# Kernel tuning notes

Measured on AMD Instinct MI355X. Metric: run time of the kernel, lower is better.

Reference implementation:

```python
import jax, jax.numpy as jnp
import numpy as np

N_EMBD = 1024
HEAD_SIZE = 64


def setup_inputs() -> dict:
    key = jax.random.key(0)
    kx, kq, kk, kv = jax.random.split(key, 4)
    B, T = 8, 2048
    x = jax.random.normal(kx, (B, T, N_EMBD), dtype=jnp.float32)
    s = 1.0 / np.sqrt(N_EMBD)
    Wq = jax.random.normal(kq, (N_EMBD, HEAD_SIZE), dtype=jnp.float32) * s
    Wk = jax.random.normal(kk, (N_EMBD, HEAD_SIZE), dtype=jnp.float32) * s
    Wv = jax.random.normal(kv, (N_EMBD, HEAD_SIZE), dtype=jnp.float32) * s
    return {"x": x, "Wq": Wq, "Wk": Wk, "Wv": Wv}


def reference(x, Wq, Wk, Wv):
    # x: [B, T, C]; W*: [C, H]
    q = jnp.einsum('btc,ch->bth', x, Wq)
    k = jnp.einsum('btc,ch->bth', x, Wk)
    v = jnp.einsum('btc,ch->bth', x, Wv)
    H = q.shape[-1]
    score = jnp.einsum('bth,bsh->bts', q, k) / jnp.sqrt(jnp.asarray(H, q.dtype))
    T = score.shape[-1]
    causal = jnp.tril(jnp.ones((T, T), dtype=bool))  # [T, T]
    score = jnp.where(causal, score, -jnp.inf)
    attn = jax.nn.softmax(score, axis=-1)
    return jnp.einsum('bts,bsh->bth', attn, v)
```

## Files before the change

kernel.cpp:

```cpp
#include <hip/hip_runtime.h>

typedef __bf16 bf16;
typedef __attribute__((ext_vector_type(8))) __bf16 bf16x8;
typedef __attribute__((ext_vector_type(4))) __bf16 bf16x4;
typedef __attribute__((ext_vector_type(4))) float floatx4;

#define MFMA16(a, b, c) __builtin_amdgcn_mfma_f32_16x16x32_bf16((a), (b), (c), 0, 0, 0)

__global__ void prep_w(const float* __restrict__ Wq, const float* __restrict__ Wk,
                       const float* __restrict__ Wv, bf16* __restrict__ wTf) {
    int tid = blockIdx.x * 256 + threadIdx.x;
    int j = tid & 7;
    int l = (tid >> 3) & 15;
    int q = (tid >> 7) & 3;
    int kc = (tid >> 9) & 31;
    int mt = tid >> 14;
    int mat = mt >> 2;
    int h = ((mt & 3) << 4) + l;
    int c = kc * 32 + q * 8 + j;
    const float* W = (mat == 0) ? Wq : (mat == 1) ? Wk : Wv;
    wTf[tid] = (bf16)W[c * 64 + h];
}

__global__ __launch_bounds__(256, 2) void proj_qkv(const float* __restrict__ x,
                                                   const bf16* __restrict__ wTf,
                                                   bf16* __restrict__ q,
                                                   bf16* __restrict__ k,
                                                   bf16* __restrict__ vT) {
    __shared__ __align__(16) char xsb[32 * 2048];

    const int tid = threadIdx.x;
    const int lane = tid & 63;
    const int w = tid >> 6;
    const int l15 = lane & 15;
    const int quad = lane >> 4;
    const int T0 = blockIdx.x * 32;

    const int srow = tid >> 3;
    const int scg = tid & 7;
    const float* sg = x + (size_t)(T0 + srow) * 1024 + scg * 8;
    char* sld = xsb + srow * 2048;
    const int sws = (srow & 7) << 4;

#define STC(c, f0, f1)                                                          \
    {                                                                            \
        bf16x8 pk;                                                               \
        pk[0] = (bf16)(f0)[0]; pk[1] = (bf16)(f0)[1];                            \
        pk[2] = (bf16)(f0)[2]; pk[3] = (bf16)(f0)[3];                            \
        pk[4] = (bf16)(f1)[0]; pk[5] = (bf16)(f1)[1];                            \
        pk[6] = (bf16)(f1)[2]; pk[7] = (bf16)(f1)[3];                            \
        *(bf16x8*)(sld + (((c) * 128 + scg * 16) ^ sws)) = pk;                   \
    }

    floatx4 A0 = *(const floatx4*)(sg);
    floatx4 A1 = *(const floatx4*)(sg + 4);
    floatx4 B0 = *(const floatx4*)(sg + 64);
    floatx4 B1 = *(const floatx4*)(sg + 68);
    floatx4 C0 = *(const floatx4*)(sg + 128);
    floatx4 C1 = *(const floatx4*)(sg + 132);
    STC(0, A0, A1);
    __syncthreads();

    floatx4 acc[6] = {};
    const bf16* aw0 = wTf + (size_t)(w * 3 + 0) * 16384 + lane * 8;
    const bf16* aw1 = wTf + (size_t)(w * 3 + 1) * 16384 + lane * 8;
    const bf16* aw2 = wTf + (size_t)(w * 3 + 2) * 16384 + lane * 8;
    const char* xr = xsb + l15 * 2048;
    const int sx = (l15 & 7) << 4;
    const int q16 = quad * 16;

    bf16x8 a0c = *(const bf16x8*)(aw0);
    bf16x8 a1c = *(const bf16x8*)(aw1);
    bf16x8 a2c = *(const bf16x8*)(aw2);
    bf16x8 a0n = *(const bf16x8*)(aw0 + 512);
    bf16x8 a1n = *(const bf16x8*)(aw1 + 512);
    bf16x8 a2n = *(const bf16x8*)(aw2 + 512);

    #pragma unroll
    for (int c = 0; c < 16; c++) {
        floatx4 N0 = {}, N1 = {};
        if (c < 13) {
            N0 = *(const floatx4*)(sg + (c + 3) * 64);
            N1 = *(const floatx4*)(sg + (c + 3) * 64 + 4);
        }
        #pragma unroll
        for (int u = 0; u < 2; u++) {
            const int kc = 2 * c + u;
            bf16x8 p0 = *(const bf16x8*)(aw0 + (kc + 2) * 512);
            bf16x8 p1 = *(const bf16x8*)(aw1 + (kc + 2) * 512);
            bf16x8 p2 = *(const bf16x8*)(aw2 + (kc + 2) * 512);
            const int o = (kc * 64 + q16) ^ sx;
            bf16x8 b0 = *(const bf16x8*)(xr + o);
            bf16x8 b1 = *(const bf16x8*)(xr + 32768 + o);
            acc[0] = MFMA16(a0c, b0, acc[0]);
            acc[1] = MFMA16(a0c, b1, acc[1]);
            acc[2] = MFMA16(a1c, b0, acc[2]);
            acc[3] = MFMA16(a1c, b1, acc[3]);
            acc[4] = MFMA16(a2c, b0, acc[4]);
            acc[5] = MFMA16(a2c, b1, acc[5]);
            a0c = a0n; a1c = a1n; a2c = a2n;
            a0n = p0;  a1n = p1;  a2n = p2;
        }
        if (c < 15) STC(c + 1, B0, B1);
        __syncthreads();
        B0 = C0; B1 = C1; C0 = N0; C1 = N1;
    }
#undef STC

    #pragma unroll
    for (int i = 0; i < 3; i++) {
        int mtile = w * 3 + i;
        int mat = mtile >> 2;
        int hbase = ((mtile & 3) << 4) + (quad << 2);
        float sc = (mat == 0) ? 0.18033688011112042f : 1.0f;
        #pragma unroll
        for (int tt = 0; tt < 2; tt++) {
            const int t = T0 + tt * 16 + l15;
            floatx4 av = acc[i * 2 + tt];
            bf16x4 pk;
            pk[0] = (bf16)(av[0] * sc);
            pk[1] = (bf16)(av[1] * sc);
            pk[2] = (bf16)(av[2] * sc);
            pk[3] = (bf16)(av[3] * sc);
            if (mat == 0) {
                *(bf16x4*)(q + (size_t)t * 64 + hbase) = pk;
            } else if (mat == 1) {
                *(bf16x4*)(k + (size_t)t * 64 + hbase) = pk;
            } else {
                int bidx = t >> 11, tmod = t & 2047;
                #pragma unroll
                for (int r = 0; r < 4; r++)
                    vT[(size_t)(bidx * 64 + hbase + r) * 2048 + tmod] = pk[r];
            }
        }
    }
}

#define KP2 72
#define OH 68

__global__ __launch_bounds__(512, 4) void flash(const bf16* __restrict__ q,
                                                const bf16* __restrict__ k,
                                                const bf16* __restrict__ vT,
                                                float* __restrict__ out) {
    __shared__ char smem[8 * 16 * OH * 4];
    __shared__ float Ms[8][16], Ls[8][16];
    bf16* psall = (bf16*)smem;
    float* Os = (float*)smem;

    const int b = blockIdx.x & 7;
    const int p = blockIdx.x >> 3;
    const int t0A = p * 16;
    const int t0B = (127 - p) * 16;
    const int nttA = (p >> 2) + 1;
    const int nttB = ((127 - p) >> 2) + 1;
    const int L = nttA + nttB;

    const int tid = threadIdx.x;
    const int w = tid >> 6;
    const int lane = tid & 63;
    const int l15 = lane & 15;
    const int quad = lane >> 4;

    const int s0 = (L * w) >> 3;
    const int s1 = (L * (w + 1)) >> 3;

    const bf16* kbase = k + (size_t)(b * 2048 + l15) * 64 + quad * 8;
    const bf16* vbase = vT + (size_t)(b * 64 + l15) * 2048 + quad * 8;
    bf16* psw = psall + w * 16 * KP2;

    const bf16* qpA = q + (size_t)(b * 2048 + t0A + l15) * 64 + quad * 8;
    const bf16* qpB = q + (size_t)(b * 2048 + t0B + l15) * 64 + quad * 8;

    floatx4 oA[4] = {}, oB[4] = {};
    float miA = -1e30f, liA = 0.f, miB = -1e30f, liB = 0.f;

#define KV_STEP(jtv, isdiag, t0v, qf0v, qf1v, mi_, li_, o_)                          \
    {                                                                                 \
        const bf16* kp = kbase + (size_t)(jtv) * 4096;                                \
        floatx4 stt[4];                                                               \
        __builtin_amdgcn_s_setprio(1);                                                \
        _Pragma("unroll") for (int mt = 0; mt < 4; mt++) {                            \
            floatx4 z = {};                                                           \
            bf16x8 ka0 = *(const bf16x8*)(kp + mt * 1024);                            \
            bf16x8 ka1 = *(const bf16x8*)(kp + mt * 1024 + 32);                       \
            z = MFMA16(ka0, qf0v, z);                                                 \
            z = MFMA16(ka1, qf1v, z);                                                 \
            stt[mt] = z;                                                              \
        }                                                                             \
        __builtin_amdgcn_s_setprio(0);                                                \
        if (isdiag) {                                                                 \
            _Pragma("unroll") for (int mt = 0; mt < 4; mt++)                          \
                _Pragma("unroll") for (int r = 0; r < 4; r++) {                       \
                    int kv = (jtv) * 64 + mt * 16 + quad * 4 + r;                     \
                    if (kv > (t0v) + l15) stt[mt][r] = -1e30f;                        \
                }                                                                     \
        }                                                                             \
        float m0_ = fmaxf(fmaxf(stt[0][0], stt[0][1]), stt[0][2]);                    \
        float m1_ = fmaxf(fmaxf(stt[0][3], stt[1][0]), stt[1][1]);                    \
        float m2_ = fmaxf(fmaxf(stt[1][2], stt[1][3]), stt[2][0]);                    \
        float m3_ = fmaxf(fmaxf(stt[2][1], stt[2][2]), stt[2][3]);                    \
        float m4_ = fmaxf(fmaxf(stt[3][0], stt[3][1]), stt[3][2]);                    \
        float mx = fmaxf(fmaxf(fmaxf(m0_, m1_), m2_),                                 \
                         fmaxf(fmaxf(m3_, m4_), stt[3][3]));                          \
        mx = fmaxf(mx, __shfl_xor(mx, 16, 64));                                       \
        mx = fmaxf(mx, __shfl_xor(mx, 32, 64));                                       \
        const bool nodefer = !__all(mx - mi_ <= 8.0f);                                \
        const float mnew = nodefer ? fmaxf(mi_, mx) : mi_;                            \
        float rs = 0.f;                                                               \
        _Pragma("unroll") for (int mt = 0; mt < 4; mt++)                              \
            _Pragma("unroll") for (int r = 0; r < 4; r++) {                           \
                float pv = __builtin_amdgcn_exp2f(stt[mt][r] - mnew);                 \
                stt[mt][r] = pv;                                                      \
                rs += pv;                                                             \
            }                                                                         \
        rs += __shfl_xor(rs, 16, 64);                                                 \
        rs += __shfl_xor(rs, 32, 64);                                                 \
        if (nodefer) {                                                                \
            const float aa = __builtin_amdgcn_exp2f(mi_ - mnew);                      \
            mi_ = mnew;                                                               \
            li_ *= aa;                                                                \
            _Pragma("unroll") for (int mt = 0; mt < 4; mt++)                          \
                _Pragma("unroll") for (int r = 0; r < 4; r++) o_[mt][r] *= aa;        \
        }                                                                             \
        li_ += rs;                                                                    \
        _Pragma("unroll") for (int mt = 0; mt < 4; mt++) {                            \
            bf16x4 pk;                                                                \
            pk[0] = (bf16)stt[mt][0]; pk[1] = (bf16)stt[mt][1];                       \
            pk[2] = (bf16)stt[mt][2]; pk[3] = (bf16)stt[mt][3];                       \
            *(bf16x4*)(psw + l15 * KP2 + mt * 16 + quad * 4) = pk;                    \
        }                                                                             \
        const bf16* vp = vbase + (jtv) * 64;                                          \
        __builtin_amdgcn_s_setprio(1);                                                \
        _Pragma("unroll") for (int kc = 0; kc < 2; kc++) {                            \
            bf16x8 pb = *(const bf16x8*)(psw + l15 * KP2 + kc * 32 + quad * 8);       \
            _Pragma("unroll") for (int mt = 0; mt < 4; mt++) {                        \
                bf16x8 va = *(const bf16x8*)(vp + mt * 32768 + kc * 32);              \
                o_[mt] = MFMA16(va, pb, o_[mt]);                                      \
            }                                                                         \
        }                                                                             \
        __builtin_amdgcn_s_setprio(0);                                                \
    }

    {
        const int eA = (s1 < nttA) ? s1 : nttA;
        if (s0 < eA) {
            bf16x8 qf0 = *(const bf16x8*)qpA;
            bf16x8 qf1 = *(const bf16x8*)(qpA + 32);
            for (int s = s0; s < eA; s++) {
                KV_STEP(s, (s == nttA - 1), t0A, qf0, qf1, miA, liA, oA);
            }
        }
    }
    {
        const int sB = (s0 > nttA) ? s0 : nttA;
        if (sB < s1) {
            bf16x8 qf0 = *(const bf16x8*)qpB;
            bf16x8 qf1 = *(const bf16x8*)(qpB + 32);
            for (int s = sB; s < s1; s++) {
                KV_STEP(s - nttA, (s == L - 1), t0B, qf0, qf1, miB, liB, oB);
            }
        }
    }

    #pragma unroll
    for (int tile = 0; tile < 2; tile++) {
        __syncthreads();
        float mi = tile ? miB : miA;
        float li = tile ? liB : liA;
        if (lane < 16) { Ms[w][lane] = mi; Ls[w][lane] = li; }
        #pragma unroll
        for (int mt = 0; mt < 4; mt++) {
            floatx4 ov = tile ? oB[mt] : oA[mt];
            *(floatx4*)(Os + (w * 16 + l15) * OH + mt * 16 + quad * 4) = ov;
        }
        __syncthreads();
        {
            int qq = tid >> 5;
            int h2 = (tid & 31) * 2;
            float Mg = -1e30f;
            #pragma unroll
            for (int u = 0; u < 8; u++) Mg = fmaxf(Mg, Ms[u][qq]);
            float Lg = 0.f, v0 = 0.f, v1 = 0.f;
            #pragma unroll
            for (int u = 0; u < 8; u++) {
                float sw = __builtin_amdgcn_exp2f(Ms[u][qq] - Mg);
                Lg += sw * Ls[u][qq];
                const float* Or = Os + (u * 16 + qq) * OH + h2;
                v0 += sw * Or[0];
                v1 += sw * Or[1];
            }
            float inv = 1.0f / Lg;
            int t0v = tile ? t0B : t0A;
            float* op = out + (size_t)(b * 2048 + t0v + qq) * 64 + h2;
            op[0] = v0 * inv;
            op[1] = v1 * inv;
        }
    }
#undef KV_STEP
}

extern "C" void kernel_launch(void* const* d_in, const int* in_sizes, int n_in,
                              void* d_out, int out_size, void* d_ws, size_t ws_size,
                              hipStream_t stream) {
    const float* x  = (const float*)d_in[0];
    const float* Wq = (const float*)d_in[1];
    const float* Wk = (const float*)d_in[2];
    const float* Wv = (const float*)d_in[3];
    float* out = (float*)d_out;

    char* ws = (char*)d_ws;
    bf16* wTf = (bf16*)ws;
    bf16* q   = (bf16*)(ws + 397312);
    bf16* k   = (bf16*)(ws + 397312 + 2097152);
    bf16* vT  = (bf16*)(ws + 397312 + 2 * 2097152);

    hipLaunchKernelGGL(prep_w,   dim3(768), dim3(256), 0, stream, Wq, Wk, Wv, wTf);
    hipLaunchKernelGGL(proj_qkv, dim3(512), dim3(256), 0, stream, x, wTf, q, k, vT);
    hipLaunchKernelGGL(flash,    dim3(512), dim3(512), 0, stream, q, k, vT, out);
}
```

Measured before the change: 144.1 us.

## Stage projection x tile in two halves instead of sixteen synced chunks

The QKV projection kernel used to stream x into shared memory one 64-column chunk at a time, with a __syncthreads per chunk (16 barriers). It now issues all global loads up front into registers (64 floats per thread), stores the first half, runs 16 MFMA k-steps, then stores the second half and runs the remaining 16. This cuts barriers from sixteen to two and puts more loads in flight at once. The cost is much higher register pressure, which under launch_bounds(256,2) may cause spills, and less overlap between the global loads and the first compute phase.

Measured after the change: 140.5 us. 1.03x faster.

```diff
diff --git a/kernel.cpp b/kernel.cpp
--- a/kernel.cpp
+++ b/kernel.cpp
@@ -36,29 +36,44 @@
     const int quad = lane >> 4;
     const int T0 = blockIdx.x * 32;
 
-    const int srow = tid >> 3;
-    const int scg = tid & 7;
-    const float* sg = x + (size_t)(T0 + srow) * 1024 + scg * 8;
-    char* sld = xsb + srow * 2048;
-    const int sws = (srow & 7) << 4;
-
-#define STC(c, f0, f1)                                                          \
+    const int r = tid >> 4;
+    const int cm = tid & 15;
+    const float* g0 = x + (size_t)(T0 + r) * 1024 + cm * 8;
+    const float* g1 = x + (size_t)(T0 + r + 16) * 1024 + cm * 8;
+    char* ld0 = xsb + r * 2048;
+    char* ld1 = xsb + (r + 16) * 2048;
+    const int sws = (r & 7) << 4;
+
+#define STC8(ldb, c, f0, f1)                                                    \
     {                                                                            \
         bf16x8 pk;                                                               \
         pk[0] = (bf16)(f0)[0]; pk[1] = (bf16)(f0)[1];                            \
         pk[2] = (bf16)(f0)[2]; pk[3] = (bf16)(f0)[3];                            \
         pk[4] = (bf16)(f1)[0]; pk[5] = (bf16)(f1)[1];                            \
         pk[6] = (bf16)(f1)[2]; pk[7] = (bf16)(f1)[3];                            \
-        *(bf16x8*)(sld + (((c) * 128 + scg * 16) ^ sws)) = pk;                   \
-    }
-
-    floatx4 A0 = *(const floatx4*)(sg);
-    floatx4 A1 = *(const floatx4*)(sg + 4);
-    floatx4 B0 = *(const floatx4*)(sg + 64);
-    floatx4 B1 = *(const floatx4*)(sg + 68);
-    floatx4 C0 = *(const floatx4*)(sg + 128);
-    floatx4 C1 = *(const floatx4*)(sg + 132);
-    STC(0, A0, A1);
+        *(bf16x8*)((ldb) + ((cm * 16 + (c) * 256) ^ sws)) = pk;                  \
+    }
+
+    floatx4 fA[8], fB[8], hA[8], hB[8];
+    #pragma unroll
+    for (int c = 0; c < 4; c++) {
+        fA[2*c]   = *(const floatx4*)(g0 + c * 128);
+        fA[2*c+1] = *(const floatx4*)(g0 + c * 128 + 4);
+        fB[2*c]   = *(const floatx4*)(g1 + c * 128);
+        fB[2*c+1] = *(const floatx4*)(g1 + c * 128 + 4);
+    }
+    #pragma unroll
+    for (int c = 0; c < 4; c++) {
+        hA[2*c]   = *(const floatx4*)(g0 + 512 + c * 128);
+        hA[2*c+1] = *(const floatx4*)(g0 + 512 + c * 128 + 4);
+        hB[2*c]   = *(const floatx4*)(g1 + 512 + c * 128);
+        hB[2*c+1] = *(const floatx4*)(g1 + 512 + c * 128 + 4);
+    }
+    #pragma unroll
+    for (int c = 0; c < 4; c++) {
+        STC8(ld0, c, fA[2*c], fA[2*c+1]);
+        STC8(ld1, c, fB[2*c], fB[2*c+1]);
+    }
     __syncthreads();
 
     floatx4 acc[6] = {};
@@ -76,36 +91,38 @@
     bf16x8 a1n = *(const bf16x8*)(aw1 + 512);
     bf16x8 a2n = *(const bf16x8*)(aw2 + 512);
 
-    #pragma unroll
-    for (int c = 0; c < 16; c++) {
-        floatx4 N0 = {}, N1 = {};
-        if (c < 13) {
-            N0 = *(const floatx4*)(sg + (c + 3) * 64);
-            N1 = *(const floatx4*)(sg + (c + 3) * 64 + 4);
-        }
-        #pragma unroll
-        for (int u = 0; u < 2; u++) {
-            const int kc = 2 * c + u;
-            bf16x8 p0 = *(const bf16x8*)(aw0 + (kc + 2) * 512);
-            bf16x8 p1 = *(const bf16x8*)(aw1 + (kc + 2) * 512);
-            bf16x8 p2 = *(const bf16x8*)(aw2 + (kc + 2) * 512);
-            const int o = (kc * 64 + q16) ^ sx;
-            bf16x8 b0 = *(const bf16x8*)(xr + o);
-            bf16x8 b1 = *(const bf16x8*)(xr + 32768 + o);
-            acc[0] = MFMA16(a0c, b0, acc[0]);
-            acc[1] = MFMA16(a0c, b1, acc[1]);
-            acc[2] = MFMA16(a1c, b0, acc[2]);
-            acc[3] = MFMA16(a1c, b1, acc[3]);
-            acc[4] = MFMA16(a2c, b0, acc[4]);
-            acc[5] = MFMA16(a2c, b1, acc[5]);
-            a0c = a0n; a1c = a1n; a2c = a2n;
-            a0n = p0;  a1n = p1;  a2n = p2;
-        }
-        if (c < 15) STC(c + 1, B0, B1);
-        __syncthreads();
-        B0 = C0; B1 = C1; C0 = N0; C1 = N1;
-    }
-#undef STC
+#define KBODY(kc)                                                               \
+    {                                                                            \
+        bf16x8 p0 = *(const bf16x8*)(aw0 + ((kc) + 2) * 512);                    \
+        bf16x8 p1 = *(const bf16x8*)(aw1 + ((kc) + 2) * 512);                    \
+        bf16x8 p2 = *(const bf16x8*)(aw2 + ((kc) + 2) * 512);                    \
+        const int o = ((kc) * 64 + q16) ^ sx;                                    \
+        bf16x8 b0 = *(const bf16x8*)(xr + o);                                    \
+        bf16x8 b1 = *(const bf16x8*)(xr + 32768 + o);                            \
+        acc[0] = MFMA16(a0c, b0, acc[0]);                                        \
+        acc[1] = MFMA16(a0c, b1, acc[1]);                                        \
+        acc[2] = MFMA16(a1c, b0, acc[2]);                                        \
+        acc[3] = MFMA16(a1c, b1, acc[3]);                                        \
+        acc[4] = MFMA16(a2c, b0, acc[4]);                                        \
+        acc[5] = MFMA16(a2c, b1, acc[5]);                                        \
+        a0c = a0n; a1c = a1n; a2c = a2n;                                         \
+        a0n = p0;  a1n = p1;  a2n = p2;                                          \
+    }
+
+    #pragma unroll 4
+    for (int kc = 0; kc < 16; kc++) KBODY(kc);
+
+    #pragma unroll
+    for (int c = 4; c < 8; c++) {
+        STC8(ld0, c, hA[2*(c-4)], hA[2*(c-4)+1]);
+        STC8(ld1, c, hB[2*(c-4)], hB[2*(c-4)+1]);
+    }
+    __syncthreads();
+
+    #pragma unroll 4
+    for (int kc = 16; kc < 32; kc++) KBODY(kc);
+#undef KBODY
+#undef STC8
 
     #pragma unroll
     for (int i = 0; i < 3; i++) {
@@ -129,8 +146,8 @@
             } else {
                 int bidx = t >> 11, tmod = t & 2047;
                 #pragma unroll
-                for (int r = 0; r < 4; r++)
-                    vT[(size_t)(bidx * 64 + hbase + r) * 2048 + tmod] = pk[r];
+                for (int rr = 0; rr < 4; rr++)
+                    vT[(size_t)(bidx * 64 + hbase + rr) * 2048 + tmod] = pk[rr];
             }
         }
     }
@@ -191,9 +208,9 @@
         __builtin_amdgcn_s_setprio(0);                                                \
         if (isdiag) {                                                                 \
             _Pragma("unroll") for (int mt = 0; mt < 4; mt++)                          \
-                _Pragma("unroll") for (int r = 0; r < 4; r++) {                       \
-                    int kv = (jtv) * 64 + mt * 16 + quad * 4 + r;                     \
-                    if (kv > (t0v) + l15) stt[mt][r] = -1e30f;                        \
+                _Pragma("unroll") for (int rr = 0; rr < 4; rr++) {                    \
+                    int kv = (jtv) * 64 + mt * 16 + quad * 4 + rr;                    \
+                    if (kv > (t0v) + l15) stt[mt][rr] = -1e30f;                       \
                 }                                                                     \
         }                                                                             \
         float m0_ = fmaxf(fmaxf(stt[0][0], stt[0][1]), stt[0][2]);                    \
@@ -209,9 +226,9 @@
         const float mnew = nodefer ? fmaxf(mi_, mx) : mi_;                            \
         float rs = 0.f;                                                               \
         _Pragma("unroll") for (int mt = 0; mt < 4; mt++)                              \
-            _Pragma("unroll") for (int r = 0; r < 4; r++) {                           \
-                float pv = __builtin_amdgcn_exp2f(stt[mt][r] - mnew);                 \
-                stt[mt][r] = pv;                                                      \
+            _Pragma("unroll") for (int rr = 0; rr < 4; rr++) {                        \
+                float pv = __builtin_amdgcn_exp2f(stt[mt][rr] - mnew);                \
+                stt[mt][rr] = pv;                                                     \
                 rs += pv;                                                             \
             }                                                                         \
         rs += __shfl_xor(rs, 16, 64);                                                 \
@@ -221,7 +238,7 @@
             mi_ = mnew;                                                               \
             li_ *= aa;                                                                \
             _Pragma("unroll") for (int mt = 0; mt < 4; mt++)                          \
-                _Pragma("unroll") for (int r = 0; r < 4; r++) o_[mt][r] *= aa;        \
+                _Pragma("unroll") for (int rr = 0; rr < 4; rr++) o_[mt][rr] *= aa;    \
         }                                                                             \
         li_ += rs;                                                                    \
         _Pragma("unroll") for (int mt = 0; mt < 4; mt++) {                            \
```
